# Optimization experiments

Hardware: AMD Instinct MI355X
Metric: run time of the kernel (lower is better)

The kernel has to match this reference:

```python
import jax, jax.numpy as jnp
import numpy as np

B, T, D = 1024, 256, 256
H, L, K = 768, 6, 10          # hidden_dim, levels, conv_size
CH = H // L                   # chunk_size
GDIM = 4 * H + 2 * L          # gate projection width


def setup_inputs() -> dict:
    key = jax.random.key(0)
    ks = jax.random.split(key, 10)
    s = lambda n: 1.0 / np.sqrt(n).astype(np.float32)
    return {
        "x": jax.random.normal(ks[0], (B, T, D), jnp.float32),
        "time": jax.random.uniform(ks[1], (B, T), jnp.float32),
        "kernel_w": jax.random.normal(ks[2], (GDIM, D + 1), jnp.float32) * s(D + 1),
        "kernel_b": jnp.zeros((GDIM,), jnp.float32),
        "rec_w": jax.random.normal(ks[3], (GDIM, H + 1), jnp.float32) * s(H + 1),
        "rec_b": jnp.zeros((GDIM,), jnp.float32),
        "scale_w": jax.random.normal(ks[4], (H // 6, H), jnp.float32) * s(H),
        "scale_b": jnp.zeros((H // 6,), jnp.float32),
        "rescale_w": jax.random.normal(ks[5], (H, H // 6), jnp.float32) * s(H // 6),
        "rescale_b": jnp.zeros((H,), jnp.float32),
        "conv_w": jax.random.normal(ks[6], (H, H, K), jnp.float32) * s(H * K),
        "conv_b": jnp.zeros((H,), jnp.float32),
        "out_w": jax.random.normal(ks[7], (1, H), jnp.float32) * s(H),
        "out_b": jnp.zeros((1,), jnp.float32),
    }


def _cumax_l2r(v):
    return jnp.cumsum(jax.nn.softmax(v, axis=-1), axis=-1)


def _cumax_r2l(v):
    v = jnp.flip(v, -1)
    v = jnp.cumsum(jax.nn.softmax(v, axis=-1), axis=-1)
    return jnp.flip(v, -1)


def reference(x, time, kernel_w, kernel_b, rec_w, rec_b, scale_w, scale_b,
              rescale_w, rescale_b, conv_w, conv_b, out_w, out_b):
    b = x.shape[0]

    def step(carry, xs):
        c, h, tmp_h, tmp_dis = carry
        x_t, t_t = xs                              # [b,D], [b]
        xi = jnp.concatenate([x_t, t_t[:, None]], -1)
        hi = jnp.concatenate([h, t_t[:, None]], -1)
        g = xi @ kernel_w.T + kernel_b + hi @ rec_w.T + rec_b   # [b, 4H+2L]
        f_m = _cumax_l2r(g[:, :L])[:, :, None]                  # [b,L,1]
        i_m = _cumax_r2l(g[:, L:2 * L])[:, :, None]             # [b,L,1]
        rest = g[:, 2 * L:].reshape(b, 4 * L, CH)
        f_g = jax.nn.sigmoid(rest[:, :L])
        i_g = jax.nn.sigmoid(rest[:, L:2 * L])
        o_g = jax.nn.sigmoid(rest[:, 2 * L:3 * L])
        c_in = jnp.tanh(rest[:, 3 * L:])
        c_last = c.reshape(b, L, CH)
        ov = f_m * i_m
        c_new3 = ov * (f_g * c_last + i_g * c_in) + (f_m - ov) * c_last + (i_m - ov) * c_in
        h_new = (o_g * jnp.tanh(c_new3)).reshape(b, H)
        c_new = c_new3.reshape(b, H)
        dist = 1.0 - jnp.mean(f_m[..., 0], axis=-1)             # [b]
        tmp_h = jnp.concatenate([tmp_h[1:], h_new[None]], 0)    # sliding window [K,b,H]
        tmp_dis = jnp.concatenate([tmp_dis[1:], dist[None]], 0) # [K,b]
        return (c_new, h_new, tmp_h, tmp_dis), dist

    init = (jnp.zeros((b, H), x.dtype), jnp.zeros((b, H), x.dtype),
            jnp.zeros((K, b, H), x.dtype), jnp.zeros((K, b), x.dtype))
    xs = (jnp.transpose(x, (1, 0, 2)), time.T)
    (c_f, h_last, tmp_h, tmp_dis), distance = jax.lax.scan(step, init, xs)

    local_dis = jax.nn.softmax(jnp.cumsum(tmp_dis.T, axis=1), axis=1)    # [b,K]
    local_h = jnp.transpose(tmp_h, (1, 2, 0)) * local_dis[:, None, :]    # [b,H,K]
    theme = jax.nn.sigmoid(
        jax.nn.relu(jnp.mean(local_h, -1) @ scale_w.T + scale_b) @ rescale_w.T + rescale_b)
    conv = jnp.einsum('bhk,ohk->bo', local_h, conv_w) + conv_b           # Conv1d -> length-1 output
    rnn_out = theme * conv + h_last
    output = jax.nn.sigmoid((rnn_out @ out_w.T + out_b).reshape(b))
    return output, distance
```

## Files before the change

### kernel.cpp

```cpp
#include <hip/hip_runtime.h>
#include <hip/hip_bf16.h>
#include <math.h>
#include <stdint.h>

#define BATCH 1024
#define TT    256
#define DD    256
#define HH    768
#define LL    6
#define KCONV 10
#define CHW   128
#define KPACK 1024
#define G4    3072
#define BNT   192
#define GSTR  196

#define NSLOT   8
#define SLOT    17408
#define NS      (NSLOT * SLOT)
#define ML_OFF  52224
#define BIAS_OFF 139264
#define SMEM_SZ 140928

typedef __attribute__((ext_vector_type(8))) __bf16 bf16x8;
typedef __attribute__((ext_vector_type(4))) float f32x4;

__device__ __forceinline__ float sigf(float v) { return 1.0f / (1.0f + expf(-v)); }

#define SEL6(a, l) ((l)==0?a[0]:(l)==1?a[1]:(l)==2?a[2]:(l)==3?a[3]:(l)==4?a[4]:a[5])

__device__ __forceinline__ void gload16(const void* g, void* l) {
    __builtin_amdgcn_global_load_lds(
        (const __attribute__((address_space(1))) unsigned int*)g,
        (__attribute__((address_space(3))) unsigned int*)l, 16, 0, 0);
}
__device__ __forceinline__ void gload16_nc(const void* g, void* l) {
    __builtin_amdgcn_global_load_lds(
        (const __attribute__((address_space(1))) unsigned int*)g,
        (__attribute__((address_space(3))) unsigned int*)l, 16, 0, 0x11);
}

__device__ __forceinline__ unsigned short bf16bits(float v) {
    __hip_bfloat16 h(v);
    return *(unsigned short*)&h;
}

#define WAITV(a, b) do { \
    if (tid < 64) asm volatile("s_waitcnt vmcnt(" #a ")" ::: "memory"); \
    else          asm volatile("s_waitcnt vmcnt(" #b ")" ::: "memory"); \
} while (0)

__global__ __launch_bounds__(256) void prep_w4(
    const float* __restrict__ kw, const float* __restrict__ kb,
    const float* __restrict__ rw, const float* __restrict__ rb,
    __hip_bfloat16* __restrict__ W4, float* __restrict__ bias4, float* __restrict__ tco4)
{
    int n = blockIdx.x;
    int e = n >> 2, q = n & 3;
    int orig = 2 * LL + q * HH + e;
    int tid = threadIdx.x;
#pragma unroll
    for (int k = 0; k < 4; ++k) {
        int col = tid + k * 256;
        float v = (col < DD) ? kw[(size_t)orig * (DD + 1) + col]
                             : rw[(size_t)orig * (HH + 1) + (col - DD)];
        W4[(size_t)n * KPACK + col] = __hip_bfloat16(v);
    }
    if (tid == 0) {
        bias4[n] = kb[orig] + rb[orig];
        tco4[n]  = kw[(size_t)orig * (DD + 1) + DD] + rw[(size_t)orig * (HH + 1) + HH];
    }
}

__global__ __launch_bounds__(256) void prep_wm(
    const float* __restrict__ kw, const float* __restrict__ kb,
    const float* __restrict__ rw, const float* __restrict__ rb,
    __hip_bfloat16* __restrict__ Wm, float* __restrict__ mbias, float* __restrict__ mtco)
{
    int j = blockIdx.x;
    int tid = threadIdx.x;
#pragma unroll
    for (int k = 0; k < 4; ++k) {
        int col = tid + k * 256;
        float v = 0.0f;
        if (j < 12)
            v = (col < DD) ? kw[(size_t)j * (DD + 1) + col]
                           : rw[(size_t)j * (HH + 1) + (col - DD)];
        Wm[(size_t)j * KPACK + col] = __hip_bfloat16(v);
    }
    if (tid == 0 && j < 12) {
        mbias[j] = kb[j] + rb[j];
        mtco[j]  = kw[(size_t)j * (DD + 1) + DD] + rw[(size_t)j * (HH + 1) + HH];
    }
}

__global__ __launch_bounds__(256) void cvt_kernel(
    const float* __restrict__ src, __hip_bfloat16* __restrict__ dst, int n)
{
    int i = blockIdx.x * 256 + threadIdx.x;
    if (i < n) dst[i] = __hip_bfloat16(src[i]);
}

__global__ __launch_bounds__(256) void xcvt_kernel(
    const float* __restrict__ x, __hip_bfloat16* __restrict__ xb)
{
    size_t o = ((size_t)blockIdx.x * 256 + threadIdx.x) * 8;
    int t = (int)(o >> 18);
    int b = (int)(o >> 8) & 1023;
    int d = (int)(o & 255);
    const float* src = x + ((size_t)b * TT + t) * DD + d;
    float4 a = *(const float4*)src;
    float4 c = *(const float4*)(src + 4);
    unsigned short tmp[8];
    tmp[0] = bf16bits(a.x); tmp[1] = bf16bits(a.y);
    tmp[2] = bf16bits(a.z); tmp[3] = bf16bits(a.w);
    tmp[4] = bf16bits(c.x); tmp[5] = bf16bits(c.y);
    tmp[6] = bf16bits(c.z); tmp[7] = bf16bits(c.w);
    *(uint4*)((char*)xb + o * 2) = *(const uint4*)tmp;
}

__global__ __launch_bounds__(512, 1) void persist_kernel(
    __hip_bfloat16* __restrict__ Hb0,
    __hip_bfloat16* __restrict__ Hb1,
    const __hip_bfloat16* __restrict__ xb,
    const float* __restrict__ timep,
    const __hip_bfloat16* __restrict__ W4,
    const __hip_bfloat16* __restrict__ Wm,
    const float* __restrict__ bias4, const float* __restrict__ tco4,
    const float* __restrict__ mbias, const float* __restrict__ mtco,
    float* __restrict__ hwin,
    float* __restrict__ distp,
    unsigned* __restrict__ cnt)
{
    __shared__ __align__(16) char smem[SMEM_SZ];
    float* gl    = (float*)smem;
    float* ml    = (float*)(smem + ML_OFF);
    float* biasL = (float*)(smem + BIAS_OFF);
    float* tcoL  = biasL + 192;
    float* mbL   = tcoL + 192;
    float* mtL   = mbL + 16;

    const int tid = threadIdx.x;
    const int bid = blockIdx.x;
    const int swz = (bid & 7) * 32 + (bid >> 3);
    const int bm = swz & 15;
    const int bn = swz >> 4;

    const int lane = tid & 63;
    const int wid  = tid >> 6;
    const int wr   = wid >> 2, wc = wid & 3;
    const int kg   = lane >> 4;
    const int r15  = lane & 15;
    const bool domast = (wid == 3) || (wid == 4);
    const int r  = tid >> 3;
    const int qq = tid & 7;
    const int b  = bm * 64 + r;
    unsigned* cntg = cnt + bm * 64;

    if (tid < 192) { biasL[tid] = bias4[bn * BNT + tid]; tcoL[tid] = tco4[bn * BNT + tid]; }
    if (tid >= 256 && tid < 268) { mbL[tid - 256] = mbias[tid - 256]; mtL[tid - 256] = mtco[tid - 256]; }
    __syncthreads();

    float cst[6] = {0.f, 0.f, 0.f, 0.f, 0.f, 0.f};

    const int rowA = tid >> 2, kcA = tid & 3;
    const int swA  = kcA ^ ((rowA >> 1) & 3);
    const size_t aXoff = ((size_t)(bm * 64 + rowA) * DD + swA * 8) * 2;
    const size_t aHoff = ((size_t)(bm * 64 + rowA) * HH + swA * 8) * 2;
    const int aLds = tid * 16;
    auto bptr = [&](int cb) -> const char* {
        int row = cb >> 2, kc = cb & 3;
        int sw = kc ^ ((row >> 1) & 3);
        const __hip_bfloat16* src = (row < BNT)
            ? W4 + (size_t)(bn * BNT + row) * KPACK + sw * 8
            : Wm + (size_t)(row - BNT) * KPACK + sw * 8;
        return (const char*)src;
    };
    const char* bsrc0 = (tid >= 256) ? bptr(tid - 256) : (const char*)W4;
    const char* bsrc1 = bptr(tid + 256);
    const char* bsrc2 = (tid < 64) ? bptr(tid + 768) : (const char*)W4;
    const int bLds0 = 4096 + (tid - 256) * 16;
    const int bLds1 = 4096 + (tid + 256) * 16;
    const int bLds2 = 4096 + (tid + 768) * 16;

    int aOff[2], bOff[3];
#pragma unroll
    for (int m = 0; m < 2; ++m) {
        int ar = wr * 32 + m * 16 + r15;
        aOff[m] = (ar * 32 + ((kg ^ ((ar >> 1) & 3)) * 8)) * 2;
    }
#pragma unroll
    for (int n = 0; n < 3; ++n) {
        int br = wc * 48 + n * 16 + r15;
        bOff[n] = 4096 + (br * 32 + ((kg ^ ((br >> 1) & 3)) * 8)) * 2;
    }
    const int mrr = BNT + r15;
    const int mOff = 4096 + (mrr * 32 + ((kg ^ ((mrr >> 1) & 3)) * 8)) * 2;

    const char* hb0c = (const char*)Hb0;
    const char* hb1c = (const char*)Hb1;
    const char* xbt  = (const char*)xb;

    const char* pxA = xbt + aXoff;
    const char* phA = hb0c + aHoff;

    auto stage = [&](int slotOff, int tile) {
        const int toff = tile * 64;
        if (tid < 256) {
            if (tile < 8) gload16(pxA + toff, smem + slotOff + aLds);
            else          gload16_nc(phA + (toff - 512), smem + slotOff + aLds);
        } else {
            gload16(bsrc0 + toff, smem + slotOff + bLds0);
        }
        gload16(bsrc1 + toff, smem + slotOff + bLds1);
        if (tid < 64) gload16(bsrc2 + toff, smem + slotOff + bLds2);
    };

    stage(0 * SLOT, 0); stage(1 * SLOT, 1); stage(2 * SLOT, 2);
    stage(3 * SLOT, 3); stage(4 * SLOT, 4); stage(5 * SLOT, 5);

    for (int t = 0; t < TT; ++t) {
        const char* hbb = (t & 1) ? hb1c : hb0c;
        __hip_bfloat16* hbW = (t & 1) ? Hb0 : Hb1;
        phA = hbb + aHoff;

        f32x4 acc[2][3], accm[2];
#pragma unroll
        for (int m = 0; m < 2; ++m) {
#pragma unroll
            for (int n = 0; n < 3; ++n) acc[m][n] = (f32x4){0.f, 0.f, 0.f, 0.f};
            accm[m] = (f32x4){0.f, 0.f, 0.f, 0.f};
        }

        auto compute = [&](int slotOff) {
            const char* base = smem + slotOff;
            bf16x8 af[2], bv[3];
#pragma unroll
            for (int m = 0; m < 2; ++m) af[m] = *(const bf16x8*)(base + aOff[m]);
#pragma unroll
            for (int n = 0; n < 3; ++n) bv[n] = *(const bf16x8*)(base + bOff[n]);
            __builtin_amdgcn_s_setprio(1);
#pragma unroll
            for (int m = 0; m < 2; ++m)
#pragma unroll
                for (int n = 0; n < 3; ++n)
                    acc[m][n] = __builtin_amdgcn_mfma_f32_16x16x32_bf16(
                        af[m], bv[n], acc[m][n], 0, 0, 0);
            if (domast) {
                bf16x8 bmf = *(const bf16x8*)(base + mOff);
#pragma unroll
                for (int m = 0; m < 2; ++m)
                    accm[m] = __builtin_amdgcn_mfma_f32_16x16x32_bf16(
                        af[m], bmf, accm[m], 0, 0, 0);
            }
            __builtin_amdgcn_s_setprio(0);
        };

        WAITV(12, 8);
        __builtin_amdgcn_s_barrier();
        stage(6 * SLOT, 6); stage(7 * SLOT, 7);
        compute(0 * SLOT); compute(1 * SLOT);

        if (t > 0 && tid == 0) {
            unsigned target = (unsigned)t * 16u;
            while (__hip_atomic_load(cntg, __ATOMIC_RELAXED, __HIP_MEMORY_SCOPE_AGENT) < target)
                __builtin_amdgcn_s_sleep(1);
        }

        int c0 = 2 * SLOT;
        int s0 = 0;
#pragma unroll 1
        for (int it = 2; it < 32; it += 2) {
            if (it <= 26)      WAITV(12, 8);
            else if (it == 28) WAITV(6, 4);
            else { asm volatile("s_waitcnt vmcnt(0)" ::: "memory"); }
            __builtin_amdgcn_s_barrier();
            int c1 = c0 + SLOT; if (c1 >= NS) c1 -= NS;
            if (it <= 24) {
                int s1 = s0 + SLOT; if (s1 >= NS) s1 -= NS;
                stage(s0, it + 6); stage(s1, it + 7);
                s0 = s1 + SLOT; if (s0 >= NS) s0 -= NS;
            }
            compute(c0); compute(c1);
            c0 = c1 + SLOT; if (c0 >= NS) c0 -= NS;
        }
        __syncthreads();

#pragma unroll
        for (int m = 0; m < 2; ++m)
#pragma unroll
            for (int n = 0; n < 3; ++n) {
                int col = wc * 48 + n * 16 + r15;
                int rw0 = wr * 32 + m * 16 + kg * 4;
#pragma unroll
                for (int j = 0; j < 4; ++j)
                    gl[(rw0 + j) * GSTR + col] = acc[m][n][j];
            }
        if (domast) {
#pragma unroll
            for (int m = 0; m < 2; ++m) {
                int rw0 = wr * 32 + m * 16 + kg * 4;
#pragma unroll
                for (int j = 0; j < 4; ++j)
                    ml[(rw0 + j) * 16 + r15] = accm[m][j];
            }
        }
        __syncthreads();

        const float tv = timep[(size_t)b * TT + t];

        float mv[12];
#pragma unroll
        for (int i2 = 0; i2 < 12; ++i2)
            mv[i2] = ml[r * 16 + i2] + mbL[i2] + tv * mtL[i2];

        float mxf = mv[0], mxi = mv[6];
#pragma unroll
        for (int i2 = 1; i2 < 6; ++i2) { mxf = fmaxf(mxf, mv[i2]); mxi = fmaxf(mxi, mv[6 + i2]); }
        float fr[6], ir[6];
        float sf = 0.f, si = 0.f;
#pragma unroll
        for (int i2 = 0; i2 < 6; ++i2) {
            fr[i2] = expf(mv[i2] - mxf);     sf += fr[i2];
            ir[i2] = expf(mv[6 + i2] - mxi); si += ir[i2];
        }
        float fm[6], im[6];
        float rsf = 1.0f / sf, rsi = 1.0f / si;
        fm[0] = fr[0] * rsf;
#pragma unroll
        for (int i2 = 1; i2 < 6; ++i2) fm[i2] = fm[i2 - 1] + fr[i2] * rsf;
        im[5] = ir[5] * rsi;
#pragma unroll
        for (int i2 = 4; i2 >= 0; --i2) im[i2] = im[i2 + 1] + ir[i2] * rsi;

        if (bn == 0 && qq == 0) {
            float dist = 1.0f - (fm[0] + fm[1] + fm[2] + fm[3] + fm[4] + fm[5]) * (1.0f / 6.0f);
            distp[(size_t)t * BATCH + b] = dist;
        }

        const int e0 = bn * 48 + qq * 6;
        const int l0 = e0 >> 7, l1 = (e0 + 5) >> 7;
        const float fmA = SEL6(fm, l0), imA = SEL6(im, l0);
        const float fmB = SEL6(fm, l1), imB = SEL6(im, l1);

        const bool wh = (t >= TT - KCONV);
        float* hw = hwin + (size_t)(t % KCONV) * BATCH * HH + (size_t)b * HH;

        unsigned short hsv[6];
#pragma unroll
        for (int j = 0; j < 6; ++j) {
            int el = qq * 6 + j;
            int e  = bn * 48 + el;
            f32x4 gv = *(const f32x4*)&gl[r * GSTR + el * 4];
            float fg = sigf(gv[0] + biasL[el * 4 + 0] + tv * tcoL[el * 4 + 0]);
            float ig = sigf(gv[1] + biasL[el * 4 + 1] + tv * tcoL[el * 4 + 1]);
            float og = sigf(gv[2] + biasL[el * 4 + 2] + tv * tcoL[el * 4 + 2]);
            float ci = tanhf(gv[3] + biasL[el * 4 + 3] + tv * tcoL[el * 4 + 3]);
            float cl = cst[j];
            bool hi = (e >> 7) != l0;
            float fmv = hi ? fmB : fmA;
            float imv = hi ? imB : imA;
            float ov = fmv * imv;
            float cn = ov * (fg * cl + ig * ci) + (fmv - ov) * cl + (imv - ov) * ci;
            float hn = og * tanhf(cn);
            cst[j] = cn;
            hsv[j] = bf16bits(hn);
            if (wh) hw[e] = hn;
        }
        {
            unsigned w0 = (unsigned)hsv[0] | ((unsigned)hsv[1] << 16);
            unsigned w1 = (unsigned)hsv[2] | ((unsigned)hsv[3] << 16);
            unsigned w2 = (unsigned)hsv[4] | ((unsigned)hsv[5] << 16);
            uint64_t ad = (uint64_t)(uintptr_t)(hbW + (size_t)b * HH + e0);
            asm volatile(
                "global_store_dword %0, %1, off sc0 sc1\n\t"
                "global_store_dword %0, %2, off offset:4 sc0 sc1\n\t"
                "global_store_dword %0, %3, off offset:8 sc0 sc1"
                :: "v"(ad), "v"(w0), "v"(w1), "v"(w2) : "memory");
        }
        __syncthreads();

        xbt += (size_t)BATCH * DD * 2;
        pxA = xbt + aXoff;
        if (t + 1 < TT) {
            asm volatile("s_waitcnt vmcnt(0)" ::: "memory");
            if (tid == 0)
                __hip_atomic_fetch_add(cntg, 1u, __ATOMIC_RELAXED, __HIP_MEMORY_SCOPE_AGENT);
            stage(0 * SLOT, 0); stage(1 * SLOT, 1); stage(2 * SLOT, 2);
            stage(3 * SLOT, 3); stage(4 * SLOT, 4); stage(5 * SLOT, 5);
        }
    }
}

template <int SPLIT>
__global__ __launch_bounds__(256, 2) void gemm_mfma(
    const __hip_bfloat16* __restrict__ A, int lda,
    const __hip_bfloat16* __restrict__ W, int ldw,
    float* __restrict__ C, int ldc, size_t cstride, int Kdim, int nbm, int nbn)
{
    __shared__ unsigned short As[2][64 * 64];
    __shared__ unsigned short Bs[2][128 * 64];

    const int nwg = nbm * nbn * SPLIT;
    const int cpx = nwg >> 3;
    const int bid = blockIdx.x;
    const int swz = (bid & 7) * cpx + (bid >> 3);
    const int z   = swz % SPLIT;
    const int t2  = swz / SPLIT;
    const int bm  = t2 % nbm;
    const int bn  = t2 / nbm;
    const int kspan = Kdim / SPLIT;

    const int tid  = threadIdx.x;
    const int lane = tid & 63;
    const int wid  = tid >> 6;
    const int wr   = wid >> 1, wc = wid & 1;
    const int kg   = lane >> 4;
    const int r15  = lane & 15;

    f32x4 acc[2][4];
#pragma unroll
    for (int m = 0; m < 2; ++m)
#pragma unroll
        for (int n = 0; n < 4; ++n) acc[m][n] = (f32x4){0.f, 0.f, 0.f, 0.f};

    const __hip_bfloat16* Abase = A + (size_t)(bm * 64) * lda + (size_t)z * kspan;
    const __hip_bfloat16* Wbase = W + (size_t)(bn * 128) * ldw + (size_t)z * kspan;

    auto stage = [&](int buf, int k0) {
        unsigned short* Ad = &As[buf][0];
        unsigned short* Bd = &Bs[buf][0];
#pragma unroll
        for (int i = 0; i < 2; ++i) {
            int c = tid + i * 256;
            int row = c >> 3, kc = c & 7;
            gload16(Abase + (size_t)row * lda + k0 + ((kc ^ (row & 7)) * 8), Ad + c * 8);
        }
#pragma unroll
        for (int i = 0; i < 4; ++i) {
            int c = tid + i * 256;
            int row = c >> 3, kc = c & 7;
            gload16(Wbase + (size_t)row * ldw + k0 + ((kc ^ (row & 7)) * 8), Bd + c * 8);
        }
    };

    const int NIT = kspan / 64;
    stage(0, 0);
    int cur = 0;
    for (int it = 0; it < NIT; ++it) {
        if (it + 1 < NIT) {
            stage(cur ^ 1, (it + 1) * 64);
            asm volatile("s_waitcnt vmcnt(6)" ::: "memory");
        } else {
            asm volatile("s_waitcnt vmcnt(0)" ::: "memory");
        }
        __builtin_amdgcn_s_barrier();

#pragma unroll
        for (int ks = 0; ks < 2; ++ks) {
            const int kb = ks * 4 + kg;
            bf16x8 af[2], bv[4];
#pragma unroll
            for (int m = 0; m < 2; ++m) {
                int ar = wr * 32 + m * 16 + r15;
                af[m] = *(const bf16x8*)&As[cur][ar * 64 + ((kb ^ (ar & 7)) * 8)];
            }
#pragma unroll
            for (int n = 0; n < 4; ++n) {
                int br = wc * 64 + n * 16 + r15;
                bv[n] = *(const bf16x8*)&Bs[cur][br * 64 + ((kb ^ (br & 7)) * 8)];
            }
#pragma unroll
            for (int m = 0; m < 2; ++m)
#pragma unroll
                for (int n = 0; n < 4; ++n)
                    acc[m][n] = __builtin_amdgcn_mfma_f32_16x16x32_bf16(
                        af[m], bv[n], acc[m][n], 0, 0, 0);
        }
        __builtin_amdgcn_s_barrier();
        cur ^= 1;
    }

    float* Cp = C + (size_t)z * cstride;
    const int crow0 = bm * 64 + wr * 32 + (lane >> 4) * 4;
    const int ccol0 = bn * 128 + wc * 64 + r15;
#pragma unroll
    for (int m = 0; m < 2; ++m)
#pragma unroll
        for (int n = 0; n < 4; ++n)
#pragma unroll
            for (int j = 0; j < 4; ++j)
                Cp[(size_t)(crow0 + m * 16 + j) * ldc + ccol0 + n * 16] = acc[m][n][j];
}

#define BM 64
#define BN 64
#define BK 32
template <int MODE>
__global__ __launch_bounds__(256) void gemm_nt(
    const float* __restrict__ A, int lda,
    const float* __restrict__ W, int ldw,
    const float* __restrict__ bias,
    float* __restrict__ C, int ldc, int M, int N, int Kdim)
{
    __shared__ float As[BK][BM + 4];
    __shared__ float Ws[BK][BN + 4];
    const int tid = threadIdx.x;
    const int bm = blockIdx.y * BM;
    const int bn = blockIdx.x * BN;
    const int tx = tid & 15;
    const int ty = tid >> 4;

    float acc[4][4];
#pragma unroll
    for (int i = 0; i < 4; ++i)
#pragma unroll
        for (int j = 0; j < 4; ++j) acc[i][j] = 0.0f;

    for (int k0 = 0; k0 < Kdim; k0 += BK) {
#pragma unroll
        for (int i = 0; i < (BM * BK) / 256; ++i) {
            int linear = tid + i * 256;
            int r = linear >> 5, kk = linear & 31;
            As[kk][r] = A[(size_t)(bm + r) * lda + k0 + kk];
        }
#pragma unroll
        for (int i = 0; i < (BN * BK) / 256; ++i) {
            int linear = tid + i * 256;
            int r = linear >> 5, kk = linear & 31;
            int gcol = bn + r;
            Ws[kk][r] = (gcol < N) ? W[(size_t)gcol * ldw + k0 + kk] : 0.0f;
        }
        __syncthreads();
#pragma unroll
        for (int kk = 0; kk < BK; ++kk) {
            float4 a4 = *(const float4*)&As[kk][ty * 4];
            float4 b4 = *(const float4*)&Ws[kk][tx * 4];
            float av[4] = {a4.x, a4.y, a4.z, a4.w};
            float bv[4] = {b4.x, b4.y, b4.z, b4.w};
#pragma unroll
            for (int i = 0; i < 4; ++i)
#pragma unroll
                for (int j = 0; j < 4; ++j)
                    acc[i][j] = fmaf(av[i], bv[j], acc[i][j]);
        }
        __syncthreads();
    }
#pragma unroll
    for (int i = 0; i < 4; ++i) {
        int row = bm + ty * 4 + i;
#pragma unroll
        for (int j = 0; j < 4; ++j) {
            int col = bn + tx * 4 + j;
            if (col < N) {
                float v = acc[i][j] + bias[col];
                if (MODE == 2) v = fmaxf(v, 0.0f);
                if (MODE == 3) v = sigf(v);
                C[(size_t)row * ldc + col] = v;
            }
        }
    }
}

__global__ __launch_bounds__(256) void window_kernel(
    const float* __restrict__ dist_out, float* __restrict__ ld)
{
    int b = blockIdx.x * blockDim.x + threadIdx.x;
    if (b >= BATCH) return;
    float w[KCONV];
    float run = 0.0f, m = -1e30f;
#pragma unroll
    for (int k = 0; k < KCONV; ++k) {
        run += dist_out[(size_t)(TT - KCONV + k) * BATCH + b];
        w[k] = run;
        m = fmaxf(m, run);
    }
    float s = 0.0f;
#pragma unroll
    for (int k = 0; k < KCONV; ++k) { w[k] = expf(w[k] - m); s += w[k]; }
    float inv = 1.0f / s;
#pragma unroll
    for (int k = 0; k < KCONV; ++k) ld[b * KCONV + k] = w[k] * inv;
}

__global__ __launch_bounds__(256) void localh_kernel(
    const float* __restrict__ hwin, const float* __restrict__ ld,
    __hip_bfloat16* __restrict__ Lhb, float* __restrict__ mh)
{
    int idx = blockIdx.x * 256 + threadIdx.x;
    int b = idx / HH;
    int e = idx - b * HH;
    float lv[KCONV];
#pragma unroll
    for (int k = 0; k < KCONV; ++k) lv[k] = ld[b * KCONV + k];
    float sum = 0.0f;
#pragma unroll
    for (int k = 0; k < KCONV; ++k) {
        int slot = (TT - KCONV + k) % KCONV;
        float v = hwin[(size_t)slot * BATCH * HH + (size_t)b * HH + e] * lv[k];
        Lhb[(size_t)b * (HH * KCONV) + e * KCONV + k] = __hip_bfloat16(v);
        sum += v;
    }
    mh[idx] = sum * (1.0f / KCONV);
}

__global__ __launch_bounds__(256) void out_kernel(
    const float* __restrict__ theme, const float* __restrict__ convp, size_t cstride,
    const float* __restrict__ conv_b, const float* __restrict__ hbuf,
    const float* __restrict__ out_w, const float* __restrict__ out_b,
    float* __restrict__ out)
{
    __shared__ float red[256];
    int b = blockIdx.x;
    float p = 0.0f;
    for (int e = threadIdx.x; e < HH; e += 256) {
        float cv = conv_b[e];
#pragma unroll
        for (int zz = 0; zz < 2; ++zz)
            cv += convp[(size_t)zz * cstride + (size_t)b * HH + e];
        p += (theme[(size_t)b * HH + e] * cv + hbuf[(size_t)b * HH + e]) * out_w[e];
    }
    red[threadIdx.x] = p;
    __syncthreads();
    for (int s = 128; s > 0; s >>= 1) {
        if (threadIdx.x < s) red[threadIdx.x] += red[threadIdx.x + s];
        __syncthreads();
    }
    if (threadIdx.x == 0) out[b] = sigf(red[0] + out_b[0]);
}

extern "C" void kernel_launch(void* const* d_in, const int* in_sizes, int n_in,
                              void* d_out, int out_size, void* d_ws, size_t ws_size,
                              hipStream_t stream)
{
    const float* x       = (const float*)d_in[0];
    const float* timep   = (const float*)d_in[1];
    const float* kw      = (const float*)d_in[2];
    const float* kb      = (const float*)d_in[3];
    const float* rw      = (const float*)d_in[4];
    const float* rb      = (const float*)d_in[5];
    const float* scale_w = (const float*)d_in[6];
    const float* scale_b = (const float*)d_in[7];
    const float* resc_w  = (const float*)d_in[8];
    const float* resc_b  = (const float*)d_in[9];
    const float* conv_w  = (const float*)d_in[10];
    const float* conv_b  = (const float*)d_in[11];
    const float* out_w   = (const float*)d_in[12];
    const float* out_b   = (const float*)d_in[13];

    float* outp  = (float*)d_out;
    float* distp = outp + BATCH;

    char* cur = (char*)d_ws;
    auto carve = [&](size_t bytes) {
        char* p = cur;
        cur += (bytes + 255) & ~(size_t)255;
        return (void*)p;
    };
    __hip_bfloat16* W4     = (__hip_bfloat16*)carve((size_t)G4 * KPACK * 2);
    __hip_bfloat16* Wm     = (__hip_bfloat16*)carve((size_t)16 * KPACK * 2);
    __hip_bfloat16* xb     = (__hip_bfloat16*)carve((size_t)TT * BATCH * DD * 2);
    __hip_bfloat16* Hb0    = (__hip_bfloat16*)carve((size_t)BATCH * HH * 2);
    __hip_bfloat16* Hb1    = (__hip_bfloat16*)carve((size_t)BATCH * HH * 2);
    __hip_bfloat16* Lhb    = (__hip_bfloat16*)carve((size_t)BATCH * HH * KCONV * 2);
    __hip_bfloat16* convwb = (__hip_bfloat16*)carve((size_t)HH * HH * KCONV * 2);
    float* bias4 = (float*)carve(G4 * 4);
    float* tco4  = (float*)carve(G4 * 4);
    float* mbias = (float*)carve(64);
    float* mtco  = (float*)carve(64);
    unsigned* cnt = (unsigned*)carve(4096);
    float* hwin  = (float*)carve((size_t)KCONV * BATCH * HH * 4);
    float* ld    = (float*)carve((size_t)BATCH * KCONV * 4);
    float* mh    = (float*)carve((size_t)BATCH * HH * 4);
    float* s1    = (float*)carve((size_t)BATCH * CHW * 4);
    float* theme = (float*)carve((size_t)BATCH * HH * 4);
    float* convp = (float*)carve(2 * (size_t)BATCH * HH * 4);

    hipMemsetAsync(cnt, 0, 4096, stream);
    hipMemsetAsync(Hb0, 0, (size_t)BATCH * HH * 2, stream);
    prep_w4<<<G4, 256, 0, stream>>>(kw, kb, rw, rb, W4, bias4, tco4);
    prep_wm<<<16, 256, 0, stream>>>(kw, kb, rw, rb, Wm, mbias, mtco);
    cvt_kernel<<<(HH * HH * KCONV + 255) / 256, 256, 0, stream>>>(
        conv_w, convwb, HH * HH * KCONV);
    xcvt_kernel<<<(TT * BATCH * DD / 8 + 255) / 256, 256, 0, stream>>>(x, xb);

    {
        void* args[] = {
            (void*)&Hb0, (void*)&Hb1, (void*)&xb, (void*)&timep,
            (void*)&W4, (void*)&Wm, (void*)&bias4, (void*)&tco4,
            (void*)&mbias, (void*)&mtco, (void*)&hwin, (void*)&distp,
            (void*)&cnt
        };
        hipLaunchCooperativeKernel((void*)persist_kernel, dim3(256), dim3(512),
                                   args, 0, stream);
    }

    window_kernel<<<(BATCH + 255) / 256, 256, 0, stream>>>(distp, ld);
    localh_kernel<<<(BATCH * HH) / 256, 256, 0, stream>>>(hwin, ld, Lhb, mh);

    gemm_mfma<2><<<16 * 6 * 2, 256, 0, stream>>>(
        Lhb, HH * KCONV, convwb, HH * KCONV, convp, HH, (size_t)BATCH * HH,
        HH * KCONV, 16, 6);
    gemm_nt<2><<<dim3(CHW / BN, BATCH / BM), 256, 0, stream>>>(
        mh, HH, scale_w, HH, scale_b, s1, CHW, BATCH, CHW, HH);
    gemm_nt<3><<<dim3(HH / BN, BATCH / BM), 256, 0, stream>>>(
        s1, CHW, resc_w, CHW, resc_b, theme, HH, BATCH, HH, CHW);

    out_kernel<<<BATCH, 256, 0, stream>>>(
        theme, convp, (size_t)BATCH * HH, conv_b,
        hwin + (size_t)((TT - 1) % KCONV) * BATCH * HH,
        out_w, out_b, outp);
}
```

Before: 4.630 ms.

## Restructure recurrent GEMM pipeline into two half-buffer ping-pong groups of four tiles

Replaces the rolling 8-slot ring with fine-grained partial vmcnt waits by a double-buffered scheme. Each group of four K-tiles is computed while the other four slots are refilled, and every group boundary uses a full vmcnt(0) wait. This cuts the barrier count and the per-iteration slot bookkeeping. The cost is coarser synchronisation: waiting on all outstanding loads can expose more memory latency, and tiles 6 and 7 are now prefetched before the step loop instead of overlapping with the first computes.

Measured after the change: 4.497 ms. 1.03x faster.

```diff
diff --git a/kernel.cpp b/kernel.cpp
--- a/kernel.cpp
+++ b/kernel.cpp
@@ -216,8 +216,8 @@
         if (tid < 64) gload16(bsrc2 + toff, smem + slotOff + bLds2);
     };
 
-    stage(0 * SLOT, 0); stage(1 * SLOT, 1); stage(2 * SLOT, 2);
-    stage(3 * SLOT, 3); stage(4 * SLOT, 4); stage(5 * SLOT, 5);
+    stage(0 * SLOT, 0); stage(1 * SLOT, 1); stage(2 * SLOT, 2); stage(3 * SLOT, 3);
+    stage(4 * SLOT, 4); stage(5 * SLOT, 5); stage(6 * SLOT, 6); stage(7 * SLOT, 7);
 
     for (int t = 0; t < TT; ++t) {
         const char* hbb = (t & 1) ? hb1c : hb0c;
@@ -258,8 +258,7 @@
 
         WAITV(12, 8);
         __builtin_amdgcn_s_barrier();
-        stage(6 * SLOT, 6); stage(7 * SLOT, 7);
-        compute(0 * SLOT); compute(1 * SLOT);
+        compute(0 * SLOT); compute(1 * SLOT); compute(2 * SLOT); compute(3 * SLOT);
 
         if (t > 0 && tid == 0) {
             unsigned target = (unsigned)t * 16u;
@@ -267,23 +266,27 @@
                 __builtin_amdgcn_s_sleep(1);
         }
 
-        int c0 = 2 * SLOT;
-        int s0 = 0;
+        asm volatile("s_waitcnt vmcnt(0)" ::: "memory");
+        __builtin_amdgcn_s_barrier();
+        stage(0 * SLOT, 8); stage(1 * SLOT, 9); stage(2 * SLOT, 10); stage(3 * SLOT, 11);
+        compute(4 * SLOT); compute(5 * SLOT); compute(6 * SLOT); compute(7 * SLOT);
+
 #pragma unroll 1
-        for (int it = 2; it < 32; it += 2) {
-            if (it <= 26)      WAITV(12, 8);
-            else if (it == 28) WAITV(6, 4);
-            else { asm volatile("s_waitcnt vmcnt(0)" ::: "memory"); }
+        for (int it = 8; it <= 24; it += 4) {
+            asm volatile("s_waitcnt vmcnt(0)" ::: "memory");
             __builtin_amdgcn_s_barrier();
-            int c1 = c0 + SLOT; if (c1 >= NS) c1 -= NS;
-            if (it <= 24) {
-                int s1 = s0 + SLOT; if (s1 >= NS) s1 -= NS;
-                stage(s0, it + 6); stage(s1, it + 7);
-                s0 = s1 + SLOT; if (s0 >= NS) s0 -= NS;
-            }
-            compute(c0); compute(c1);
-            c0 = c1 + SLOT; if (c0 >= NS) c0 -= NS;
-        }
+            const int cs = (it & 4) ? 4 * SLOT : 0;
+            const int ss = cs ^ (4 * SLOT);
+            stage(ss, it + 4); stage(ss + SLOT, it + 5);
+            stage(ss + 2 * SLOT, it + 6); stage(ss + 3 * SLOT, it + 7);
+            compute(cs); compute(cs + SLOT);
+            compute(cs + 2 * SLOT); compute(cs + 3 * SLOT);
+        }
+
+        asm volatile("s_waitcnt vmcnt(0)" ::: "memory");
+        __builtin_amdgcn_s_barrier();
+        compute(4 * SLOT); compute(5 * SLOT); compute(6 * SLOT); compute(7 * SLOT);
+
         __syncthreads();
 
 #pragma unroll
@@ -386,8 +389,8 @@
             asm volatile("s_waitcnt vmcnt(0)" ::: "memory");
             if (tid == 0)
                 __hip_atomic_fetch_add(cntg, 1u, __ATOMIC_RELAXED, __HIP_MEMORY_SCOPE_AGENT);
-            stage(0 * SLOT, 0); stage(1 * SLOT, 1); stage(2 * SLOT, 2);
-            stage(3 * SLOT, 3); stage(4 * SLOT, 4); stage(5 * SLOT, 5);
+            stage(0 * SLOT, 0); stage(1 * SLOT, 1); stage(2 * SLOT, 2); stage(3 * SLOT, 3);
+            stage(4 * SLOT, 4); stage(5 * SLOT, 5); stage(6 * SLOT, 6); stage(7 * SLOT, 7);
         }
     }
 }
```
